# Performance work log

Hardware: AMD Instinct MI355X
Metric: run time of the kernel (lower is better)

## Reference

```python
import jax, jax.numpy as jnp
import numpy as np

B, S, D, H = 2, 2048, 1024, 16
DEPTH = D // H
NEG = -1e9

def setup_inputs() -> dict:
    key = jax.random.key(0)
    k = jax.random.split(key, 4)
    return {
        "token_inputs": jax.random.normal(k[0], (B, S, D), dtype=jnp.float32),
        "mask": jnp.zeros((B, 1, 1, S), dtype=jnp.float32),
        "W_qkv": jax.random.normal(k[1], (D, 3 * D), dtype=jnp.float32) * 0.02,
        "b_qkv": jnp.zeros((3 * D,), dtype=jnp.float32),
        "W_out": jax.random.normal(k[2], (D, D), dtype=jnp.float32) * 0.02,
        "b_out": jnp.zeros((D,), dtype=jnp.float32),
    }

def reference(token_inputs, mask, W_qkv, b_qkv, W_out, b_out):
    # fused QKV projection
    qkv = token_inputs @ W_qkv + b_qkv                       # [B,S,3D]
    q, k, v = jnp.split(qkv, 3, axis=-1)                     # [B,S,D] each
    # split heads -> [B,H,S,depth]
    split = lambda x: x.reshape(B, S, H, DEPTH).transpose(0, 2, 1, 3)
    q, k, v = split(q), split(k), split(v)
    # causal additive mask: 0 on/below diagonal, -1e9 above
    causal = (1.0 - jnp.tril(jnp.ones((S, S), dtype=jnp.float32))) * NEG
    full_mask = mask + causal                                # [B,1,S,S]
    # scaled dot-product attention
    scores = jnp.einsum('bhqd,bhkd->bhqk', q, k) / jnp.sqrt(jnp.float32(DEPTH))
    scores = scores + full_mask
    attn = jax.nn.softmax(scores, axis=-1)                   # [B,H,S,S]
    ctx = jnp.einsum('bhqk,bhkd->bhqd', attn, v)             # [B,H,S,depth]
    # merge heads and final projection
    ctx = ctx.transpose(0, 2, 1, 3).reshape(B, S, D)
    return ctx @ W_out + b_out
```

## Files before the change

kernel.cpp:

```cpp
#include <hip/hip_runtime.h>
#include <hip/hip_bf16.h>

#define B_ 2
#define S_ 2048
#define D_ 1024
#define H_ 16
#define DEPTH_ 64

typedef __attribute__((ext_vector_type(4))) float f32x4;
typedef __attribute__((ext_vector_type(16))) float f32x16;
typedef __attribute__((ext_vector_type(8))) short bf16x8;
typedef __attribute__((ext_vector_type(2))) int i32x2;
typedef const __attribute__((address_space(1))) unsigned int gu32;
typedef __attribute__((address_space(3))) unsigned int lu32;

__device__ __forceinline__ void gload_lds16(const void* g, void* l) {
  __builtin_amdgcn_global_load_lds((gu32*)g, (lu32*)l, 16, 0, 0);
}

__device__ __forceinline__ short f2bf(float f) {
  union { float f; unsigned u; } v; v.f = f;
  return (short)((v.u + 0x7FFFu + ((v.u >> 16) & 1u)) >> 16);
}
__device__ __forceinline__ unsigned pk2(float lo, float hi) {
  unsigned r;
  asm("v_cvt_pk_bf16_f32 %0, %1, %2" : "=v"(r) : "v"(lo), "v"(hi));
  return r;
}
__device__ __forceinline__ i32x2 plswap(unsigned a, unsigned b) {
  return __builtin_amdgcn_permlane32_swap((int)a, (int)b, false, false);
}
#define BARRIER_RAW() do {                      \
  __builtin_amdgcn_sched_barrier(0);            \
  asm volatile("" ::: "memory");                \
  __builtin_amdgcn_s_barrier();                 \
  asm volatile("" ::: "memory");                \
  __builtin_amdgcn_sched_barrier(0);            \
} while (0)

__global__ __launch_bounds__(256) void prep_kernel(
    const float* __restrict__ X, short* __restrict__ Xb,
    const float* __restrict__ Wqkv, short* __restrict__ WqkvT,
    const float* __restrict__ Wout, short* __restrict__ WoutT) {
  __shared__ short tile[32][33];
  const int bid = blockIdx.x, tid = threadIdx.x;
  if (bid < 4096) {
    int i = bid * 256 + tid;
    const float4 v = reinterpret_cast<const float4*>(X)[i];
    short2 a, b;
    *reinterpret_cast<unsigned*>(&a) = pk2(v.x, v.y);
    *reinterpret_cast<unsigned*>(&b) = pk2(v.z, v.w);
    reinterpret_cast<short4*>(Xb)[i] = make_short4(a.x, a.y, b.x, b.y);
  } else {
    const float* W;
    short* WT;
    int N, tb;
    if (bid < 7168) { W = Wqkv; WT = WqkvT; N = 3072; tb = bid - 4096; }
    else            { W = Wout; WT = WoutT; N = 1024; tb = bid - 7168; }
    const int K = 1024;
    const int nblk = N >> 5;
    const int n0 = (tb % nblk) * 32, k0 = (tb / nblk) * 32;
    const int tx = tid & 31, ty = tid >> 5;
#pragma unroll
    for (int j = 0; j < 4; ++j)
      tile[ty + 8 * j][tx] = f2bf(W[(size_t)(k0 + ty + 8 * j) * N + n0 + tx]);
    __syncthreads();
#pragma unroll
    for (int j = 0; j < 4; ++j)
      WT[(size_t)(n0 + ty + 8 * j) * K + k0 + tx] = tile[tx][ty + 8 * j];
  }
}

template <int EPI, int BM>
__global__ __launch_bounds__(512) void gemm_bt_kernel(
    const short* __restrict__ A, const short* __restrict__ BT,
    const float* __restrict__ bias,
    short* __restrict__ Qh, short* __restrict__ Kh, short* __restrict__ VTt,
    float* __restrict__ Out, int M, int N, int K) {
  constexpr int MI = BM / 64;
  constexpr int ASZ = BM * 32;
  constexpr int BSZ = 128 * 32;
  __shared__ short smem[2 * ASZ + 2 * BSZ];
  const int nwg = gridDim.x * gridDim.y;
  int flat = blockIdx.y * gridDim.x + blockIdx.x;
  flat = (flat & 7) * (nwg >> 3) + (flat >> 3);
  const int bm = (flat / gridDim.x) * BM, bn = (flat % gridDim.x) * 128;
  const int tid = threadIdx.x;
  const int w = tid >> 6, lane = tid & 63;
  const int wr = w >> 1, wc = w & 1;
  const int lr = lane & 15, lg = lane >> 4;
  const int s_r = lane >> 2, s_c = (lane & 3) * 8;
  f32x4 acc[MI][4] = {};
  const int nk = K >> 5;

  auto stage = [&](int buf, int kt) {
    short* Asb = smem + (buf ? ASZ : 0);
    short* Bsb = smem + 2 * ASZ + (buf ? BSZ : 0);
    if (BM == 128 || w < 4)
      gload_lds16(&A[(size_t)(bm + 16 * w + s_r) * K + kt * 32 + s_c], &Asb[16 * w * 32]);
    gload_lds16(&BT[(size_t)(bn + 16 * w + s_r) * K + kt * 32 + s_c], &Bsb[16 * w * 32]);
  };

  stage(0, 0);
  asm volatile("s_waitcnt vmcnt(0)" ::: "memory");
  BARRIER_RAW();
  int cur = 0;
  for (int kt = 0; kt < nk; ++kt) {
    if (kt + 1 < nk) {
      stage(cur ^ 1, kt + 1);
      if (BM == 128 || w < 4) asm volatile("s_waitcnt vmcnt(2)" ::: "memory");
      else                    asm volatile("s_waitcnt vmcnt(1)" ::: "memory");
    } else {
      asm volatile("s_waitcnt vmcnt(0)" ::: "memory");
    }
    BARRIER_RAW();
    const short* Asb = smem + (cur ? ASZ : 0);
    const short* Bsb = smem + 2 * ASZ + (cur ? BSZ : 0);
    bf16x8 af[MI], bfr[4];
#pragma unroll
    for (int mi = 0; mi < MI; ++mi)
      af[mi] = *reinterpret_cast<const bf16x8*>(&Asb[((BM / 4) * wr + 16 * mi + lr) * 32 + 8 * lg]);
#pragma unroll
    for (int ni = 0; ni < 4; ++ni)
      bfr[ni] = *reinterpret_cast<const bf16x8*>(&Bsb[(64 * wc + 16 * ni + lr) * 32 + 8 * lg]);
#pragma unroll
    for (int mi = 0; mi < MI; ++mi)
#pragma unroll
      for (int ni = 0; ni < 4; ++ni)
        acc[mi][ni] = __builtin_amdgcn_mfma_f32_16x16x32_bf16(af[mi], bfr[ni], acc[mi][ni], 0, 0, 0);
    BARRIER_RAW();
    cur ^= 1;
  }

  if constexpr (EPI == 0) {
    if (bn >= 2 * D_) {
      __syncthreads();
      short* vt = smem;
#pragma unroll
      for (int mi = 0; mi < MI; ++mi)
#pragma unroll
        for (int ni = 0; ni < 4; ++ni)
#pragma unroll
          for (int r = 0; r < 4; r += 2) {
            int row_local = (BM / 4) * wr + 16 * mi + 4 * lg + r;
            int col_local = 64 * wc + 16 * ni + lr;
            float bv = bias[bn + col_local];
            unsigned u = pk2(acc[mi][ni][r] + bv, acc[mi][ni][r + 1] + bv);
            int rsw = row_local ^ ((col_local & 7) << 3);
            *reinterpret_cast<unsigned*>(&vt[col_local * 128 + rsw]) = u;
          }
      __syncthreads();
      const int b = bm >> 11, sbase = bm & (S_ - 1);
#pragma unroll
      for (int p = 0; p < 4; ++p) {
        int slot = 512 * p + tid;
        int vrow = slot >> 4, seg = slot & 15;
        int dd_col = bn - 2 * D_ + vrow;
        int hh = dd_col >> 6, dd = dd_col & 63;
        int csw = (seg * 8) ^ ((vrow & 7) << 3);
        short* dst = &VTt[((size_t)(b * H_ + hh) * DEPTH_ + dd) * S_ + sbase + seg * 8];
        *reinterpret_cast<bf16x8*>(dst) = *reinterpret_cast<const bf16x8*>(&vt[vrow * 128 + csw]);
      }
    } else {
      constexpr float SCQ = 0.125f * 1.44269504f;
#pragma unroll
      for (int mi = 0; mi < MI; ++mi)
#pragma unroll
        for (int ni = 0; ni < 4; ++ni)
#pragma unroll
          for (int r = 0; r < 4; ++r) {
            int row = bm + (BM / 4) * wr + 16 * mi + 4 * lg + r;
            int col = bn + 64 * wc + 16 * ni + lr;
            float v = acc[mi][ni][r] + bias[col];
            int b = row >> 11, s = row & (S_ - 1);
            int which = col >> 10, cm = col & (D_ - 1);
            int hh = cm >> 6, dd = cm & 63;
            size_t bh = (size_t)(b * H_ + hh);
            if (which == 0) Qh[(bh * S_ + s) * DEPTH_ + dd] = f2bf(v * SCQ);
            else            Kh[(bh * S_ + s) * DEPTH_ + dd] = f2bf(v);
          }
    }
  } else {
#pragma unroll
    for (int mi = 0; mi < MI; ++mi)
#pragma unroll
      for (int ni = 0; ni < 4; ++ni)
#pragma unroll
        for (int r = 0; r < 4; ++r) {
          int row = bm + (BM / 4) * wr + 16 * mi + 4 * lg + r;
          int col = bn + 64 * wc + 16 * ni + lr;
          Out[(size_t)row * N + col] = acc[mi][ni][r] + bias[col];
        }
  }
}

__global__ __launch_bounds__(256, 4) void attn_kernel(
    const short* __restrict__ Qh, const short* __restrict__ Kh,
    const short* __restrict__ VTt, const float* __restrict__ mask,
    short* __restrict__ ctx) {
  constexpr float LOG2E = 1.44269504f;
  __shared__ short smem[16384];
  const int bid = blockIdx.x;
  const int j = bid >> 5, g = j & 7, rr = j >> 3;
  const int qt = (rr == 0) ? 31 - g : (rr == 1) ? 16 + g : (rr == 2) ? 15 - g : g;
  const int bh = bid & 31;
  const int b = bh >> 4, h = bh & 15;
  const short* Qp = Qh + (size_t)bh * S_ * DEPTH_;
  const short* Kp = Kh + (size_t)bh * S_ * DEPTH_;
  const short* Vp = VTt + (size_t)bh * DEPTH_ * S_;
  const int tid = threadIdx.x;
  const int w = tid >> 6, lane = tid & 63;
  const int sw = w & 1, ch = w >> 1;
  const int lq = lane & 31, hi = lane >> 5;
  const int q0w = qt * 64 + sw * 32;
  const int scs = 8 * ((lane & 7) ^ ((lane >> 3) & 7));
  const int srw = lane >> 3;
  short* Ksc = smem + ch * 8192;
  short* Vsc = Ksc + 4096;

  bf16x8 qf[4];
#pragma unroll
  for (int ksd = 0; ksd < 4; ++ksd)
    qf[ksd] = *reinterpret_cast<const bf16x8*>(&Qp[(size_t)(q0w + lq) * DEPTH_ + 16 * ksd + 8 * hi]);

  bf16x8 ones = {};
  if (hi == 0) ones[0] = (short)0x3F80;

  f32x16 acc0 = {}, acc1 = {};
  float l_run = 0.f;

  const int nt = qt + 1;
  const int nh = (nt + 1) >> 1;
  for (int i = 0; i < nh; ++i) {
    const int kt = ch ? (nh + i) : i;
    const bool valid = kt < nt;
    const int k0 = kt * 64;
    __syncthreads();
    if (valid) {
#pragma unroll
      for (int jj = 0; jj < 4; ++jj) {
        const int brow = sw * 32 + jj * 8;
        gload_lds16(&Kp[(size_t)(k0 + brow + srw) * DEPTH_ + scs], &Ksc[brow * 64]);
        gload_lds16(&Vp[(size_t)(brow + srw) * S_ + k0 + scs], &Vsc[brow * 64]);
      }
    }
    __syncthreads();
    if (!valid) continue;

    f32x16 sc[2] = {{}, {}};
#pragma unroll
    for (int h2 = 0; h2 < 2; ++h2) {
#pragma unroll
      for (int ksd = 0; ksd < 4; ++ksd) {
        const int row = h2 * 32 + lq;
        const int col = (16 * ksd + 8 * hi) ^ ((row & 7) * 8);
        bf16x8 kf = *reinterpret_cast<const bf16x8*>(&Ksc[row * 64 + col]);
        sc[h2] = __builtin_amdgcn_mfma_f32_32x32x16_bf16(kf, qf[ksd], sc[h2], 0, 0, 0);
      }
      float mv = mask[(size_t)b * S_ + k0 + h2 * 32 + lq];
      bf16x8 maf = {};
      if (hi == 0) maf[0] = f2bf(LOG2E * mv);
      sc[h2] = __builtin_amdgcn_mfma_f32_32x32x16_bf16(maf, ones, sc[h2], 0, 0, 0);
    }
    if (kt == nt - 1) {
      const int qg = q0w + lq;
#pragma unroll
      for (int h2 = 0; h2 < 2; ++h2)
#pragma unroll
        for (int r = 0; r < 16; ++r) {
          int kvg = k0 + (r & 3) + 8 * (r >> 2) + 4 * hi + 32 * h2;
          if (kvg > qg) sc[h2][r] = -1e30f;
        }
    }
#pragma unroll
    for (int h2 = 0; h2 < 2; ++h2)
#pragma unroll
      for (int r = 0; r < 16; ++r) sc[h2][r] = exp2f(sc[h2][r]);
    float s8[8];
#pragma unroll
    for (int r = 0; r < 8; ++r) s8[r] = (sc[0][r] + sc[0][r + 8]) + (sc[1][r] + sc[1][r + 8]);
#pragma unroll
    for (int r = 0; r < 4; ++r) s8[r] = s8[r] + s8[r + 4];
    float su = (s8[0] + s8[1]) + (s8[2] + s8[3]);
    {
      union { float f; int i; } sb; sb.f = su;
      i32x2 rs = plswap((unsigned)sb.i, (unsigned)sb.i);
      union { int i; float f; } p0, p1; p0.i = rs[0]; p1.i = rs[1];
      l_run += p0.f + p1.f;
    }

#pragma unroll
    for (int h2 = 0; h2 < 2; ++h2) {
#pragma unroll
      for (int ks = 0; ks < 2; ++ks) {
        const int rb = 8 * ks;
        unsigned a = pk2(sc[h2][rb + 0], sc[h2][rb + 1]);
        unsigned bq = pk2(sc[h2][rb + 2], sc[h2][rb + 3]);
        unsigned c = pk2(sc[h2][rb + 4], sc[h2][rb + 5]);
        unsigned d = pk2(sc[h2][rb + 6], sc[h2][rb + 7]);
        i32x2 r02 = plswap(a, c);
        i32x2 r13 = plswap(bq, d);
        union { unsigned u[4]; bf16x8 v; } pf;
        pf.u[0] = (unsigned)r02[0];
        pf.u[1] = (unsigned)r13[0];
        pf.u[2] = (unsigned)r02[1];
        pf.u[3] = (unsigned)r13[1];
#pragma unroll
        for (int dh = 0; dh < 2; ++dh) {
          const int row = dh * 32 + lq;
          const int col = (32 * h2 + 16 * ks + 8 * hi) ^ ((row & 7) * 8);
          bf16x8 vf = *reinterpret_cast<const bf16x8*>(&Vsc[row * 64 + col]);
          if (dh == 0) acc0 = __builtin_amdgcn_mfma_f32_32x32x16_bf16(vf, pf.v, acc0, 0, 0, 0);
          else         acc1 = __builtin_amdgcn_mfma_f32_32x32x16_bf16(vf, pf.v, acc1, 0, 0, 0);
        }
      }
    }
  }

  __syncthreads();
  float* F  = (float*)smem;
  float* ML = (float*)(smem + 8192);
  short* ob = smem + 8704;
  if (ch == 1) {
    float* dst = F + ((size_t)sw * 64 + lane) * 32;
#pragma unroll
    for (int r = 0; r < 16; ++r) { dst[r] = acc0[r]; dst[16 + r] = acc1[r]; }
    ML[sw * 64 + lane] = l_run;
  }
  __syncthreads();
  if (ch == 0) {
    const float* src = F + ((size_t)sw * 64 + lane) * 32;
    const float rl = 1.f / (l_run + ML[sw * 64 + lane]);
#pragma unroll
    for (int r = 0; r < 16; ++r) {
      acc0[r] = (acc0[r] + src[r]) * rl;
      acc1[r] = (acc1[r] + src[16 + r]) * rl;
    }
#pragma unroll
    for (int dh = 0; dh < 2; ++dh) {
      const f32x16& Aa = dh ? acc1 : acc0;
#pragma unroll
      for (int gg = 0; gg < 4; ++gg)
#pragma unroll
        for (int p = 0; p < 2; ++p) {
          int r0 = 4 * gg + 2 * p;
          int d0 = 2 * p + 8 * gg + 4 * hi + 32 * dh;
          unsigned u = pk2(Aa[r0], Aa[r0 + 1]);
          *reinterpret_cast<unsigned*>(&ob[(sw * 32 + lq) * 72 + d0]) = u;
        }
    }
  }
  __syncthreads();
  {
    const int row = tid >> 2, seg = tid & 3;
    short* dst = ctx + ((size_t)b * S_ + qt * 64 + row) * D_ + h * 64 + seg * 16;
    const short* srcp = &ob[row * 72 + seg * 16];
    *reinterpret_cast<bf16x8*>(dst) = *reinterpret_cast<const bf16x8*>(srcp);
    *reinterpret_cast<bf16x8*>(dst + 8) = *reinterpret_cast<const bf16x8*>(srcp + 8);
  }
}

extern "C" void kernel_launch(void* const* d_in, const int* in_sizes, int n_in,
                              void* d_out, int out_size, void* d_ws, size_t ws_size,
                              hipStream_t stream) {
  const float* X    = (const float*)d_in[0];
  const float* mask = (const float*)d_in[1];
  const float* Wqkv = (const float*)d_in[2];
  const float* bqkv = (const float*)d_in[3];
  const float* Wout = (const float*)d_in[4];
  const float* bout = (const float*)d_in[5];
  float* Out = (float*)d_out;

  short* ws    = (short*)d_ws;
  short* Xb    = ws;
  short* WqkvT = Xb + (size_t)4096 * 1024;
  short* WoutT = WqkvT + (size_t)3072 * 1024;
  short* Qh    = WoutT + (size_t)1024 * 1024;
  short* Kh    = Qh + (size_t)B_ * H_ * S_ * DEPTH_;
  short* VTt   = Kh + (size_t)B_ * H_ * S_ * DEPTH_;
  short* ctx   = VTt + (size_t)B_ * H_ * S_ * DEPTH_;

  prep_kernel<<<8192, 256, 0, stream>>>(X, Xb, Wqkv, WqkvT, Wout, WoutT);
  gemm_bt_kernel<0, 128><<<dim3(24, 32), 512, 0, stream>>>(Xb, WqkvT, bqkv, Qh, Kh, VTt, nullptr,
                                                           4096, 3072, 1024);
  attn_kernel<<<1024, 256, 0, stream>>>(Qh, Kh, VTt, mask, ctx);
  gemm_bt_kernel<1, 64><<<dim3(8, 64), 512, 0, stream>>>(ctx, WoutT, bout, nullptr, nullptr, nullptr,
                                                         Out, 4096, 1024, 1024);
}
```

Baseline: 106.5 us.

## Split long causal query tiles across two blocks and merge partials

Query tiles 20-31, the longest under the causal mask, now have their KV range split across two workgroups. Each half writes unnormalized fp32 partial outputs and row sums to a scratch buffer, and a new merge kernel adds them, normalizes and writes bf16 ctx. The goal is to even out per-block work and fill the GPU better, at the cost of an extra launch and global traffic for the partials. The scratch buffer Pb aliases the start of the workspace, where Xb lives. That is safe only because Xb is no longer read after the QKV GEMM.

```diff
diff --git a/kernel.cpp b/kernel.cpp
--- a/kernel.cpp
+++ b/kernel.cpp
@@ -197,13 +197,16 @@
 __global__ __launch_bounds__(256, 4) void attn_kernel(
     const short* __restrict__ Qh, const short* __restrict__ Kh,
     const short* __restrict__ VTt, const float* __restrict__ mask,
-    short* __restrict__ ctx) {
+    short* __restrict__ ctx, float* __restrict__ Pb) {
   constexpr float LOG2E = 1.44269504f;
   __shared__ short smem[16384];
-  const int bid = blockIdx.x;
-  const int j = bid >> 5, g = j & 7, rr = j >> 3;
-  const int qt = (rr == 0) ? 31 - g : (rr == 1) ? 16 + g : (rr == 2) ? 15 - g : g;
-  const int bh = bid & 31;
+  const int bh = blockIdx.x;
+  const int y = blockIdx.y;
+  int qt, half = 0;
+  bool split = false;
+  if (y < 4)       { qt = 19 - y; }
+  else if (y < 28) { int p = (y - 4) >> 1; qt = 31 - p; half = (y - 4) & 1; split = true; }
+  else             { qt = 15 - (y - 28); }
   const int b = bh >> 4, h = bh & 15;
   const short* Qp = Qh + (size_t)bh * S_ * DEPTH_;
   const short* Kp = Kh + (size_t)bh * S_ * DEPTH_;
@@ -230,10 +233,15 @@
   float l_run = 0.f;
 
   const int nt = qt + 1;
-  const int nh = (nt + 1) >> 1;
-  for (int i = 0; i < nh; ++i) {
-    const int kt = ch ? (nh + i) : i;
-    const bool valid = kt < nt;
+  int rs, rn;
+  if (!split) { rs = 0; rn = nt; }
+  else { int h0 = (nt + 1) >> 1; rs = half ? h0 : 0; rn = half ? nt - h0 : h0; }
+  const int inner = (rn + 1) >> 1;
+  const int my0 = rs + (ch ? inner : 0);
+  const int myn = ch ? rn - inner : inner;
+  for (int i = 0; i < inner; ++i) {
+    const int kt = my0 + i;
+    const bool valid = i < myn;
     const int k0 = kt * 64;
     __syncthreads();
     if (valid) {
@@ -284,8 +292,8 @@
     float su = (s8[0] + s8[1]) + (s8[2] + s8[3]);
     {
       union { float f; int i; } sb; sb.f = su;
-      i32x2 rs = plswap((unsigned)sb.i, (unsigned)sb.i);
-      union { int i; float f; } p0, p1; p0.i = rs[0]; p1.i = rs[1];
+      i32x2 rsw2 = plswap((unsigned)sb.i, (unsigned)sb.i);
+      union { int i; float f; } p0, p1; p0.i = rsw2[0]; p1.i = rsw2[1];
       l_run += p0.f + p1.f;
     }
 
@@ -330,34 +338,75 @@
   __syncthreads();
   if (ch == 0) {
     const float* src = F + ((size_t)sw * 64 + lane) * 32;
-    const float rl = 1.f / (l_run + ML[sw * 64 + lane]);
+    const float lsum = l_run + ML[sw * 64 + lane];
 #pragma unroll
     for (int r = 0; r < 16; ++r) {
-      acc0[r] = (acc0[r] + src[r]) * rl;
-      acc1[r] = (acc1[r] + src[16 + r]) * rl;
-    }
-#pragma unroll
-    for (int dh = 0; dh < 2; ++dh) {
-      const f32x16& Aa = dh ? acc1 : acc0;
-#pragma unroll
-      for (int gg = 0; gg < 4; ++gg)
-#pragma unroll
-        for (int p = 0; p < 2; ++p) {
-          int r0 = 4 * gg + 2 * p;
-          int d0 = 2 * p + 8 * gg + 4 * hi + 32 * dh;
-          unsigned u = pk2(Aa[r0], Aa[r0 + 1]);
-          *reinterpret_cast<unsigned*>(&ob[(sw * 32 + lq) * 72 + d0]) = u;
-        }
-    }
-  }
-  __syncthreads();
-  {
+      acc0[r] += src[r];
+      acc1[r] += src[16 + r];
+    }
+    if (split) {
+      float* Pp = Pb + (size_t)(bh * 24 + (qt - 20) * 2 + half) * 4160;
+#pragma unroll
+      for (int r = 0; r < 16; ++r) {
+        int d0 = (r & 3) + 8 * (r >> 2) + 4 * hi;
+        Pp[d0 * 64 + sw * 32 + lq] = acc0[r];
+        Pp[(d0 + 32) * 64 + sw * 32 + lq] = acc1[r];
+      }
+      if (hi == 0) Pp[4096 + sw * 32 + lq] = lsum;
+    } else {
+      const float rl = 1.f / lsum;
+#pragma unroll
+      for (int dh = 0; dh < 2; ++dh) {
+        const f32x16& Aa = dh ? acc1 : acc0;
+#pragma unroll
+        for (int gg = 0; gg < 4; ++gg)
+#pragma unroll
+          for (int p = 0; p < 2; ++p) {
+            int r0 = 4 * gg + 2 * p;
+            int d0 = 2 * p + 8 * gg + 4 * hi + 32 * dh;
+            unsigned u = pk2(Aa[r0] * rl, Aa[r0 + 1] * rl);
+            *reinterpret_cast<unsigned*>(&ob[(sw * 32 + lq) * 72 + d0]) = u;
+          }
+      }
+    }
+  }
+  if (!split) {
+    __syncthreads();
     const int row = tid >> 2, seg = tid & 3;
     short* dst = ctx + ((size_t)b * S_ + qt * 64 + row) * D_ + h * 64 + seg * 16;
     const short* srcp = &ob[row * 72 + seg * 16];
     *reinterpret_cast<bf16x8*>(dst) = *reinterpret_cast<const bf16x8*>(srcp);
     *reinterpret_cast<bf16x8*>(dst + 8) = *reinterpret_cast<const bf16x8*>(srcp + 8);
   }
+}
+
+__global__ __launch_bounds__(256) void merge_kernel(const float* __restrict__ Pb,
+                                                    short* __restrict__ ctx) {
+  __shared__ float t[64][65];
+  __shared__ float linv[64];
+  const int bh = blockIdx.x & 31, qi = blockIdx.x >> 5;
+  const int b = bh >> 4, h = bh & 15;
+  const int qt = 20 + qi;
+  const float* P0 = Pb + (size_t)(bh * 24 + qi * 2) * 4160;
+  const float* P1 = P0 + 4160;
+  const int tid = threadIdx.x;
+#pragma unroll
+  for (int k = 0; k < 16; ++k) {
+    int idx = tid + 256 * k;
+    int d = idx >> 6, q = idx & 63;
+    t[q][d] = P0[idx] + P1[idx];
+  }
+  if (tid < 64) linv[tid] = 1.f / (P0[4096 + tid] + P1[4096 + tid]);
+  __syncthreads();
+  const int row = tid >> 2, seg = tid & 3;
+  const float rl = linv[row];
+  short* dst = ctx + ((size_t)b * S_ + qt * 64 + row) * D_ + h * 64 + seg * 16;
+  union { unsigned u[8]; bf16x8 v[2]; } o;
+#pragma unroll
+  for (int p = 0; p < 8; ++p)
+    o.u[p] = pk2(t[row][seg * 16 + 2 * p] * rl, t[row][seg * 16 + 2 * p + 1] * rl);
+  *reinterpret_cast<bf16x8*>(dst) = o.v[0];
+  *reinterpret_cast<bf16x8*>(dst + 8) = o.v[1];
 }
 
 extern "C" void kernel_launch(void* const* d_in, const int* in_sizes, int n_in,
@@ -379,11 +428,13 @@
   short* Kh    = Qh + (size_t)B_ * H_ * S_ * DEPTH_;
   short* VTt   = Kh + (size_t)B_ * H_ * S_ * DEPTH_;
   short* ctx   = VTt + (size_t)B_ * H_ * S_ * DEPTH_;
+  float* Pb    = (float*)ws;
 
   prep_kernel<<<8192, 256, 0, stream>>>(X, Xb, Wqkv, WqkvT, Wout, WoutT);
   gemm_bt_kernel<0, 128><<<dim3(24, 32), 512, 0, stream>>>(Xb, WqkvT, bqkv, Qh, Kh, VTt, nullptr,
                                                            4096, 3072, 1024);
-  attn_kernel<<<1024, 256, 0, stream>>>(Qh, Kh, VTt, mask, ctx);
+  attn_kernel<<<dim3(32, 44), 256, 0, stream>>>(Qh, Kh, VTt, mask, ctx, Pb);
+  merge_kernel<<<384, 256, 0, stream>>>(Pb, ctx);
   gemm_bt_kernel<1, 64><<<dim3(8, 64), 512, 0, stream>>>(ctx, WoutT, bout, nullptr, nullptr, nullptr,
                                                          Out, 4096, 1024, 1024);
 }
```

Measured after the change: 112.0 us. 1.05x slower.
